# Kernel optimization log

Measured on AMD Instinct MI355X. Metric: run time of the kernel, lower is better.

Reference implementation:

```python
import jax, jax.numpy as jnp
import numpy as np


def _gcn_conv(x, W, b, src, dst, n_nodes):
    # PyG GCNConv with add_self_loops=True, edge_weight=None (implicit ones),
    # symmetric normalization: D^{-1/2} A_hat D^{-1/2} (X W) + b
    xw = x @ W                                    # [N, H]
    loop = jnp.arange(n_nodes, dtype=src.dtype)
    src_f = jnp.concatenate([src, loop])          # [E+N]
    dst_f = jnp.concatenate([dst, loop])          # [E+N]
    w = jnp.ones(src_f.shape[0], dtype=x.dtype)
    deg = jax.ops.segment_sum(w, dst_f, num_segments=n_nodes)  # in-degree incl. self-loop
    dinv = jnp.where(deg > 0, jax.lax.rsqrt(deg), 0.0)
    norm = dinv[src_f] * dinv[dst_f]              # [E+N]
    msgs = norm[:, None] * xw[src_f]              # [E+N, H]
    out = jax.ops.segment_sum(msgs, dst_f, num_segments=n_nodes)
    return out + b


def setup_inputs() -> dict:
    key = jax.random.key(0)
    k1, k2, k3, k4 = jax.random.split(key, 4)
    N, E, D, H = 100000, 1600000, 256, 128
    x = jax.random.normal(k1, (N, D), dtype=jnp.float32)
    edge_index = jax.random.randint(k2, (2, E), 0, N, dtype=jnp.int64)
    # Glorot-scaled weights
    W1 = jax.random.normal(k3, (D, H), dtype=jnp.float32) * np.sqrt(2.0 / (D + H))
    b1 = jnp.zeros((H,), dtype=jnp.float32)
    W2 = jax.random.normal(k4, (H, 1), dtype=jnp.float32) * np.sqrt(2.0 / (H + 1))
    b2 = jnp.zeros((1,), dtype=jnp.float32)
    return {"x": x, "edge_index": edge_index, "W1": W1, "b1": b1, "W2": W2, "b2": b2}


def reference(x, edge_index, W1, b1, W2, b2):
    n_nodes = x.shape[0]
    src, dst = edge_index[0], edge_index[1]
    h = _gcn_conv(x, W1, b1, src, dst, n_nodes)   # conv1
    h = jax.nn.relu(h)                            # relu; dropout is identity in eval mode
    out = _gcn_conv(h, W2, b2, src, dst, n_nodes) # conv2 -> [N, 1]
    return out.reshape(-1)                        # x.view(-1)
```

## Files before the change

### kernel.cpp

```cpp
#include <hip/hip_runtime.h>
#include <hip/hip_fp16.h>
#include <cstdint>
#include <cstddef>


#define ELLW 64

typedef _Float16 half8 __attribute__((ext_vector_type(8)));
typedef _Float16 half2t __attribute__((ext_vector_type(2)));
typedef float floatx4 __attribute__((ext_vector_type(4)));
typedef float floatv4 __attribute__((ext_vector_type(4)));
typedef int intv4 __attribute__((ext_vector_type(4)));
typedef unsigned int uintv4 __attribute__((ext_vector_type(4)));

__global__ __launch_bounds__(256) void prep0_k(int* __restrict__ cnt,
                                               const float* __restrict__ W1,
                                               _Float16* __restrict__ wz,
                                               _Float16* __restrict__ z1h,
                                               float* __restrict__ z2w,
                                               int N, int nd) {
  int b = blockIdx.x, tid = threadIdx.x;
  if (b < nd) {
    int i = b * 256 + tid;
    if (i <= N) cnt[i] = 0;
  } else if (b < nd + 128) {
    int id = (b - nd) * 256 + tid;
    int j = id & 7, lane = (id >> 3) & 63, nb = (id >> 9) & 7, kb = id >> 12;
    int k = kb * 32 + ((lane >> 4) << 3) + j;
    int n = nb * 16 + (lane & 15);
    wz[id] = (_Float16)W1[k * 128 + n];
  } else {
    if (tid < 128) z1h[(size_t)N * 128 + tid] = (_Float16)0.f;
    if (tid == 0) z2w[N] = 0.f;
  }
}

__global__ __launch_bounds__(256) void fused_k(const float* __restrict__ X,
                                               const _Float16* __restrict__ wz,
                                               _Float16* __restrict__ z1h, int N,
                                               const int* __restrict__ src,
                                               const int* __restrict__ dst,
                                               int* __restrict__ cnt,
                                               int* __restrict__ ell, int E,
                                               int gb) {
  __shared__ char lds_raw[16 * 1024];

  if (blockIdx.x >= gb) {
    int base = ((blockIdx.x - gb) * 256 + threadIdx.x) * 8;
    if (base + 7 < E) {
      intv4 d0 = __builtin_nontemporal_load((const intv4*)(dst + base));
      intv4 d1 = __builtin_nontemporal_load((const intv4*)(dst + base + 4));
      intv4 s0 = __builtin_nontemporal_load((const intv4*)(src + base));
      intv4 s1 = __builtin_nontemporal_load((const intv4*)(src + base + 4));
      int d[8] = {d0[0], d0[1], d0[2], d0[3], d1[0], d1[1], d1[2], d1[3]};
      int s[8] = {s0[0], s0[1], s0[2], s0[3], s1[0], s1[1], s1[2], s1[3]};
      int p[8];
#pragma unroll
      for (int i = 0; i < 8; ++i) p[i] = atomicAdd(&cnt[d[i]], 1);
#pragma unroll
      for (int i = 0; i < 8; ++i)
        if (p[i] < ELLW) ell[(size_t)d[i] * ELLW + p[i]] = s[i];
    } else {
      for (int e = base; e < E && e < base + 8; ++e) {
        int dd = dst[e];
        int p = atomicAdd(&cnt[dd], 1);
        if (p < ELLW) ell[(size_t)dd * ELLW + p] = src[e];
      }
    }
    return;
  }

  _Float16* Bl = (_Float16*)lds_raw;
  _Float16* Ol = (_Float16*)lds_raw;

  int tid = threadIdx.x;
  int wave = tid >> 6, lane = tid & 63;
  int m = lane & 15, q = lane >> 4;
  int row0 = blockIdx.x * 64;
  int row = row0 + wave * 16 + m;

  floatx4 acc[8];
#pragma unroll
  for (int nb = 0; nb < 8; ++nb) acc[nb] = (floatx4)(0.f);

  const uintv4* wsrc = (const uintv4*)wz;
  uintv4* bdst = (uintv4*)Bl;

#pragma unroll
  for (int ph = 0; ph < 4; ++ph) {
    if (ph) __syncthreads();
#pragma unroll
    for (int i = 0; i < 4; ++i) bdst[i * 256 + tid] = wsrc[ph * 1024 + i * 256 + tid];
    __syncthreads();
#pragma unroll
    for (int kk = 0; kk < 2; ++kk) {
      int kb = ph * 2 + kk;
      half8 a;
      if (row < N) {
        const floatv4* ap = (const floatv4*)(X + (size_t)row * 256 + kb * 32 + q * 8);
        floatv4 a0 = __builtin_nontemporal_load(ap);
        floatv4 a1 = __builtin_nontemporal_load(ap + 1);
        a[0] = (_Float16)a0[0]; a[1] = (_Float16)a0[1];
        a[2] = (_Float16)a0[2]; a[3] = (_Float16)a0[3];
        a[4] = (_Float16)a1[0]; a[5] = (_Float16)a1[1];
        a[6] = (_Float16)a1[2]; a[7] = (_Float16)a1[3];
      } else {
#pragma unroll
        for (int j = 0; j < 8; ++j) a[j] = (_Float16)0.f;
      }
#pragma unroll
      for (int nb = 0; nb < 8; ++nb) {
        half8 b = *(const half8*)(Bl + ((size_t)(kk * 8 + nb) * 64 + lane) * 8);
        acc[nb] = __builtin_amdgcn_mfma_f32_16x16x32_f16(a, b, acc[nb], 0, 0, 0);
      }
    }
  }
  __syncthreads();

#pragma unroll
  for (int nb = 0; nb < 8; ++nb) {
    int col = nb * 16 + m;
#pragma unroll
    for (int r = 0; r < 4; ++r) {
      int orow = wave * 16 + q * 4 + r;
      Ol[orow * 128 + col] = (_Float16)acc[nb][r];
    }
  }
  __syncthreads();

  const uintv4* osrc = (const uintv4*)Ol;
  uintv4* gdst = (uintv4*)(z1h + (size_t)row0 * 128);
#pragma unroll
  for (int i = 0; i < 4; ++i) {
    int idx = i * 256 + tid;
    int r = idx >> 4;
    if (row0 + r < N) gdst[idx] = osrc[idx];
  }
}

__global__ __launch_bounds__(256) void agg1_k(const _Float16* __restrict__ z1h,
                                              const int* __restrict__ cnt,
                                              const int* __restrict__ ell,
                                              const float* __restrict__ b1,
                                              const float* __restrict__ W2,
                                              float* __restrict__ z2w, int N) {
  int d = blockIdx.x * 4 + (threadIdx.x >> 6);
  int lane = threadIdx.x & 63;
  if (d >= N) return;
  int cd = cnt[d];
  int c = min(cd, ELLW);
  int raw = __builtin_nontemporal_load(ell + (size_t)d * ELLW + lane);
  int idx = (lane < c) ? raw : N;
  float wl = rsqrtf((float)(cnt[idx] + 1));
  float dd = rsqrtf((float)(cd + 1));

  half2t self = ((const half2t*)(z1h + (size_t)d * 128))[lane];
  float ax = dd * (float)self[0];
  float ay = dd * (float)self[1];

  int cpad = (c + 15) & ~15;
  for (int e = 0; e < cpad; e += 16) {
#pragma unroll
    for (int j = 0; j < 16; ++j) {
      int s = __builtin_amdgcn_readlane(idx, e + j);
      float w = __int_as_float(__builtin_amdgcn_readlane(__float_as_int(wl), e + j));
      half2t v = ((const half2t*)(z1h + (size_t)s * 128))[lane];
      ax = fmaf(w, (float)v[0], ax);
      ay = fmaf(w, (float)v[1], ay);
    }
  }

  float2 bb = ((const float2*)b1)[lane];
  float hx = fmaxf(fmaf(dd, ax, bb.x), 0.f);
  float hy = fmaxf(fmaf(dd, ay, bb.y), 0.f);
  float2 w2 = ((const float2*)W2)[lane];
  float dot = hx * w2.x + hy * w2.y;
#pragma unroll
  for (int off = 32; off >= 1; off >>= 1) dot += __shfl_xor(dot, off, 64);
  if (lane == 0) z2w[d] = dd * dot;
}

__global__ __launch_bounds__(256) void agg2_k(const float* __restrict__ z2w,
                                              const int* __restrict__ cnt,
                                              const int* __restrict__ ell,
                                              const float* __restrict__ b2,
                                              float* __restrict__ out, int N) {
  int d = blockIdx.x * 4 + (threadIdx.x >> 6);
  int lane = threadIdx.x & 63;
  if (d >= N) return;
  int cd = cnt[d];
  int c = min(cd, ELLW);
  int raw = __builtin_nontemporal_load(ell + (size_t)d * ELLW + lane);
  int idx = (lane < c) ? raw : N;
  float v = z2w[idx];
#pragma unroll
  for (int off = 32; off >= 1; off >>= 1) v += __shfl_xor(v, off, 64);
  if (lane == 0) out[d] = rsqrtf((float)(cd + 1)) * (v + z2w[d]) + b2[0];
}

extern "C" void kernel_launch(void* const* d_in, const int* in_sizes, int n_in,
                              void* d_out, int out_size, void* d_ws, size_t ws_size,
                              hipStream_t stream) {
  (void)n_in; (void)out_size; (void)ws_size;
  const float* x = (const float*)d_in[0];
  const int* edge = (const int*)d_in[1];
  const float* W1 = (const float*)d_in[2];
  const float* b1 = (const float*)d_in[3];
  const float* W2 = (const float*)d_in[4];
  const float* b2 = (const float*)d_in[5];
  float* out = (float*)d_out;

  const int D = 256, H = 128;
  int N = in_sizes[0] / D;
  int E = in_sizes[1] / 2;
  const int* srcp = edge;
  const int* dstp = edge + E;

  char* ws = (char*)d_ws;
  size_t off = 0;
  auto alloc = [&](size_t bytes) -> void* {
    void* p = ws + off;
    off += (bytes + 255) & ~(size_t)255;
    return p;
  };
  int* cnt        = (int*)alloc((size_t)(N + 1) * 4);
  float* z2w      = (float*)alloc((size_t)(N + 1) * 4);
  int* ell        = (int*)alloc((size_t)N * ELLW * 4);
  _Float16* wz    = (_Float16*)alloc((size_t)32768 * 2);
  _Float16* z1h   = (_Float16*)alloc((size_t)(N + 1) * H * 2);

  int gb = (N + 63) / 64;
  int fb = (E + 2047) / 2048;
  int nd = (N + 256) / 256;
  prep0_k<<<dim3(nd + 128 + 1), dim3(256), 0, stream>>>(cnt, W1, wz, z1h, z2w, N, nd);
  fused_k<<<dim3(gb + fb), dim3(256), 0, stream>>>(x, wz, z1h, N, srcp, dstp, cnt, ell, E, gb);
  agg1_k<<<dim3((N + 3) / 4), dim3(256), 0, stream>>>(z1h, cnt, ell, b1, W2, z2w, N);
  agg2_k<<<dim3((N + 3) / 4), dim3(256), 0, stream>>>(z2w, cnt, ell, b2, out, N);
}
```

Baseline: 325.7 us.

## Build ELL adjacency via two-pass bucket sort overlapped with GEMM tiles

```diff
diff --git a/kernel.cpp b/kernel.cpp
--- a/kernel.cpp
+++ b/kernel.cpp
@@ -5,6 +5,9 @@
 
 
 #define ELLW 64
+#define BSH 9
+#define BNODES (1 << BSH)
+#define BPAD 16
 
 typedef _Float16 half8 __attribute__((ext_vector_type(8)));
 typedef _Float16 half2t __attribute__((ext_vector_type(2)));
@@ -13,58 +16,139 @@
 typedef int intv4 __attribute__((ext_vector_type(4)));
 typedef unsigned int uintv4 __attribute__((ext_vector_type(4)));
 
-__global__ __launch_bounds__(256) void prep0_k(int* __restrict__ cnt,
-                                               const float* __restrict__ W1,
-                                               _Float16* __restrict__ wz,
-                                               _Float16* __restrict__ z1h,
-                                               float* __restrict__ z2w,
-                                               int N, int nd) {
+__global__ __launch_bounds__(256) void prep_k(const float* __restrict__ W1,
+                                              _Float16* __restrict__ wz,
+                                              _Float16* __restrict__ z1h,
+                                              float* __restrict__ z2w,
+                                              int* __restrict__ cnt,
+                                              int* __restrict__ gcnt,
+                                              int N, int NB) {
   int b = blockIdx.x, tid = threadIdx.x;
-  if (b < nd) {
-    int i = b * 256 + tid;
-    if (i <= N) cnt[i] = 0;
-  } else if (b < nd + 128) {
-    int id = (b - nd) * 256 + tid;
+  if (b < 128) {
+    int id = b * 256 + tid;
     int j = id & 7, lane = (id >> 3) & 63, nb = (id >> 9) & 7, kb = id >> 12;
     int k = kb * 32 + ((lane >> 4) << 3) + j;
     int n = nb * 16 + (lane & 15);
     wz[id] = (_Float16)W1[k * 128 + n];
+  } else if (b == 128) {
+    if (tid < 128) z1h[(size_t)N * 128 + tid] = (_Float16)0.f;
+    if (tid == 0) { z2w[N] = 0.f; cnt[N] = 0; }
   } else {
-    if (tid < 128) z1h[(size_t)N * 128 + tid] = (_Float16)0.f;
-    if (tid == 0) z2w[N] = 0.f;
-  }
-}
-
-__global__ __launch_bounds__(256) void fused_k(const float* __restrict__ X,
+    int i = (b - 129) * 256 + tid;
+    if (i < NB * BPAD) gcnt[i] = 0;
+  }
+}
+
+__global__ __launch_bounds__(256) void stage_k(int kind, int fb, int g0,
+                                               const float* __restrict__ X,
                                                const _Float16* __restrict__ wz,
                                                _Float16* __restrict__ z1h, int N,
                                                const int* __restrict__ src,
                                                const int* __restrict__ dst,
+                                               int* __restrict__ gcnt,
+                                               int* __restrict__ gcur,
+                                               int* __restrict__ bbase,
+                                               int* __restrict__ barr,
+                                               int* __restrict__ ell,
                                                int* __restrict__ cnt,
-                                               int* __restrict__ ell, int E,
-                                               int gb) {
+                                               int E, int NB) {
   __shared__ char lds_raw[16 * 1024];
-
-  if (blockIdx.x >= gb) {
-    int base = ((blockIdx.x - gb) * 256 + threadIdx.x) * 8;
-    if (base + 7 < E) {
-      intv4 d0 = __builtin_nontemporal_load((const intv4*)(dst + base));
-      intv4 d1 = __builtin_nontemporal_load((const intv4*)(dst + base + 4));
-      intv4 s0 = __builtin_nontemporal_load((const intv4*)(src + base));
-      intv4 s1 = __builtin_nontemporal_load((const intv4*)(src + base + 4));
-      int d[8] = {d0[0], d0[1], d0[2], d0[3], d1[0], d1[1], d1[2], d1[3]};
-      int s[8] = {s0[0], s0[1], s0[2], s0[3], s1[0], s1[1], s1[2], s1[3]};
-      int p[8];
-#pragma unroll
-      for (int i = 0; i < 8; ++i) p[i] = atomicAdd(&cnt[d[i]], 1);
-#pragma unroll
-      for (int i = 0; i < 8; ++i)
-        if (p[i] < ELLW) ell[(size_t)d[i] * ELLW + p[i]] = s[i];
+  int tid = threadIdx.x;
+
+  if ((int)blockIdx.x < fb) {
+    if (kind == 0) {
+      int* bc = (int*)lds_raw;
+      for (int i = tid; i < NB; i += 256) bc[i] = 0;
+      __syncthreads();
+      int base = ((int)blockIdx.x * 256 + tid) * 16;
+#pragma unroll
+      for (int g = 0; g < 4; ++g) {
+        int b4 = base + g * 4;
+        if (b4 + 3 < E) {
+          intv4 d4 = __builtin_nontemporal_load((const intv4*)(dst + b4));
+          atomicAdd(&bc[d4[0] >> BSH], 1);
+          atomicAdd(&bc[d4[1] >> BSH], 1);
+          atomicAdd(&bc[d4[2] >> BSH], 1);
+          atomicAdd(&bc[d4[3] >> BSH], 1);
+        } else {
+          for (int e = b4; e < E && e < b4 + 4; ++e) atomicAdd(&bc[dst[e] >> BSH], 1);
+        }
+      }
+      __syncthreads();
+      for (int i = tid; i < NB; i += 256) {
+        int cc = bc[i];
+        if (cc) atomicAdd(&gcnt[i * BPAD], cc);
+      }
+    } else if (kind == 1) {
+      int* sh = (int*)lds_raw;
+      int v = (tid < NB) ? gcnt[tid * BPAD] : 0;
+      sh[tid] = v;
+      __syncthreads();
+      for (int o = 1; o < 256; o <<= 1) {
+        int t = (tid >= o) ? sh[tid - o] : 0;
+        __syncthreads();
+        sh[tid] += t;
+        __syncthreads();
+      }
+      int incl = sh[tid];
+      int excl = incl - v;
+      if (tid < NB) { bbase[tid] = excl; gcur[tid * BPAD] = excl; }
+      if (tid == NB - 1) bbase[NB] = incl;
+    } else if (kind == 2) {
+      int* bc = (int*)lds_raw;
+      int* bb = bc + 256;
+      for (int i = tid; i < NB; i += 256) bc[i] = 0;
+      __syncthreads();
+      int base = ((int)blockIdx.x * 256 + tid) * 8;
+      int dv[8], sv[8], rv[8], bkv[8];
+      int ne = 0;
+      if (base + 7 < E) {
+        intv4 d0 = __builtin_nontemporal_load((const intv4*)(dst + base));
+        intv4 d1 = __builtin_nontemporal_load((const intv4*)(dst + base + 4));
+        intv4 s0 = __builtin_nontemporal_load((const intv4*)(src + base));
+        intv4 s1 = __builtin_nontemporal_load((const intv4*)(src + base + 4));
+        dv[0] = d0[0]; dv[1] = d0[1]; dv[2] = d0[2]; dv[3] = d0[3];
+        dv[4] = d1[0]; dv[5] = d1[1]; dv[6] = d1[2]; dv[7] = d1[3];
+        sv[0] = s0[0]; sv[1] = s0[1]; sv[2] = s0[2]; sv[3] = s0[3];
+        sv[4] = s1[0]; sv[5] = s1[1]; sv[6] = s1[2]; sv[7] = s1[3];
+        ne = 8;
+      } else {
+        for (int e = base; e < E && e < base + 8; ++e) {
+          dv[ne] = dst[e]; sv[ne] = src[e]; ++ne;
+        }
+      }
+      for (int i = 0; i < ne; ++i) {
+        bkv[i] = dv[i] >> BSH;
+        rv[i] = atomicAdd(&bc[bkv[i]], 1);
+      }
+      __syncthreads();
+      for (int i = tid; i < NB; i += 256) {
+        int cc = bc[i];
+        bb[i] = cc ? atomicAdd(&gcur[i * BPAD], cc) : 0;
+      }
+      __syncthreads();
+      for (int i = 0; i < ne; ++i) {
+        unsigned dl = (unsigned)(dv[i] & (BNODES - 1));
+        barr[bb[bkv[i]] + rv[i]] = (int)((dl << 23) | (unsigned)sv[i]);
+      }
     } else {
-      for (int e = base; e < E && e < base + 8; ++e) {
-        int dd = dst[e];
-        int p = atomicAdd(&cnt[dd], 1);
-        if (p < ELLW) ell[(size_t)dd * ELLW + p] = src[e];
+      int* cl = (int*)lds_raw;
+      int bkt = (int)blockIdx.x;
+      int lo = bkt << BSH;
+      for (int i = tid; i < BNODES; i += 256) cl[i] = 0;
+      __syncthreads();
+      int e0 = bbase[bkt], e1 = bbase[bkt + 1];
+      for (int e = e0 + tid; e < e1; e += 256) {
+        unsigned v = (unsigned)barr[e];
+        int dl = (int)(v >> 23);
+        int s = (int)(v & 0x7FFFFFu);
+        int p = atomicAdd(&cl[dl], 1);
+        if (p < ELLW) ell[(size_t)(lo + dl) * ELLW + p] = s;
+      }
+      __syncthreads();
+      for (int i = tid; i < BNODES; i += 256) {
+        int node = lo + i;
+        if (node < N) cnt[node] = cl[i];
       }
     }
     return;
@@ -73,10 +157,9 @@
   _Float16* Bl = (_Float16*)lds_raw;
   _Float16* Ol = (_Float16*)lds_raw;
 
-  int tid = threadIdx.x;
   int wave = tid >> 6, lane = tid & 63;
   int m = lane & 15, q = lane >> 4;
-  int row0 = blockIdx.x * 64;
+  int row0 = (g0 + (int)blockIdx.x - fb) * 64;
   int row = row0 + wave * 16 + m;
 
   floatx4 acc[8];
@@ -204,8 +287,8 @@
   (void)n_in; (void)out_size; (void)ws_size;
   const float* x = (const float*)d_in[0];
   const int* edge = (const int*)d_in[1];
+  const float* b1 = (const float*)d_in[3];
   const float* W1 = (const float*)d_in[2];
-  const float* b1 = (const float*)d_in[3];
   const float* W2 = (const float*)d_in[4];
   const float* b2 = (const float*)d_in[5];
   float* out = (float*)d_out;
@@ -215,6 +298,7 @@
   int E = in_sizes[1] / 2;
   const int* srcp = edge;
   const int* dstp = edge + E;
+  int NB = (N + BNODES - 1) >> BSH;
 
   char* ws = (char*)d_ws;
   size_t off = 0;
@@ -228,12 +312,29 @@
   int* ell        = (int*)alloc((size_t)N * ELLW * 4);
   _Float16* wz    = (_Float16*)alloc((size_t)32768 * 2);
   _Float16* z1h   = (_Float16*)alloc((size_t)(N + 1) * H * 2);
-
-  int gb = (N + 63) / 64;
-  int fb = (E + 2047) / 2048;
-  int nd = (N + 256) / 256;
-  prep0_k<<<dim3(nd + 128 + 1), dim3(256), 0, stream>>>(cnt, W1, wz, z1h, z2w, N, nd);
-  fused_k<<<dim3(gb + fb), dim3(256), 0, stream>>>(x, wz, z1h, N, srcp, dstp, cnt, ell, E, gb);
+  int* gcnt       = (int*)alloc((size_t)NB * BPAD * 4);
+  int* gcur       = (int*)alloc((size_t)NB * BPAD * 4);
+  int* bbase      = (int*)alloc((size_t)(NB + 1) * 4);
+  int* barr       = (int*)alloc((size_t)E * 4);
+
+  int tiles = (N + 63) / 64;
+  int c = tiles / 4;
+  int c3 = tiles - 3 * c;
+  int fb0 = (E + 4095) / 4096;
+  int fb1 = 1;
+  int fb2 = (E + 2047) / 2048;
+  int fb3 = NB;
+
+  prep_k<<<dim3(129 + (NB * BPAD + 255) / 256), dim3(256), 0, stream>>>(
+      W1, wz, z1h, z2w, cnt, gcnt, N, NB);
+  stage_k<<<dim3(fb0 + c), dim3(256), 0, stream>>>(0, fb0, 0, x, wz, z1h, N,
+      srcp, dstp, gcnt, gcur, bbase, barr, ell, cnt, E, NB);
+  stage_k<<<dim3(fb1 + c), dim3(256), 0, stream>>>(1, fb1, c, x, wz, z1h, N,
+      srcp, dstp, gcnt, gcur, bbase, barr, ell, cnt, E, NB);
+  stage_k<<<dim3(fb2 + c), dim3(256), 0, stream>>>(2, fb2, 2 * c, x, wz, z1h, N,
+      srcp, dstp, gcnt, gcur, bbase, barr, ell, cnt, E, NB);
+  stage_k<<<dim3(fb3 + c3), dim3(256), 0, stream>>>(3, fb3, 3 * c, x, wz, z1h, N,
+      srcp, dstp, gcnt, gcur, bbase, barr, ell, cnt, E, NB);
   agg1_k<<<dim3((N + 3) / 4), dim3(256), 0, stream>>>(z1h, cnt, ell, b1, W2, z2w, N);
   agg2_k<<<dim3((N + 3) / 4), dim3(256), 0, stream>>>(z2w, cnt, ell, b2, out, N);
 }
```

New measurement: 323.1 us. No clear change (-0.8%).
